# Optimization experiments

Measured on AMD Instinct MI355X. Metric: run time of the kernel, lower is better.

## Reference

```python
import jax, jax.numpy as jnp
import numpy as np

EPS = 1e-6


def setup_inputs() -> dict:
    key = jax.random.key(0)
    kq, kk, kv = jax.random.split(key, 3)
    B, H, S, D = 1, 16, 2048, 64
    q = jax.random.normal(kq, (B, H, S, D), dtype=jnp.float32)
    k = jax.random.normal(kk, (B, H, S, D), dtype=jnp.float32)
    v = jax.random.normal(kv, (B, H, S, D), dtype=jnp.float32)
    return {"q": q, "k": k, "v": v}


def reference(q, k, v):
    # Rebased linear attention: squared scaled QK score, causal mask,
    # normalized by running row-sum (not softmax).
    B, H, S, D = q.shape
    scale = D ** (-0.5)
    # [B,H,S,S] raw scores
    s = jnp.einsum("bhid,bhjd->bhij", q, k) * scale
    s2 = s * s
    causal = jnp.tril(jnp.ones((S, S), dtype=bool))  # k_idx <= q_idx
    s2 = jnp.where(causal, s2, jnp.zeros((), dtype=s2.dtype))
    z = jnp.sum(s2, axis=-1)  # [B,H,S]
    o = jnp.einsum("bhij,bhjd->bhid", s2, v)
    return o / (z[..., None] + EPS)
```

## Files before the change

kernel.cpp:

```cpp
#include <hip/hip_runtime.h>

typedef __attribute__((ext_vector_type(8))) short bf16x8;
typedef __attribute__((ext_vector_type(16))) float f32x16;

#define SLEN 2048
#define DDIM 64
#define NH 16
#define KEPS 1e-6f
#define TILE_B 16384

__device__ __forceinline__ unsigned cvtpk(float lo, float hi) {
    unsigned r;
    asm("v_cvt_pk_bf16_f32 %0, %1, %2" : "=v"(r) : "v"(lo), "v"(hi));
    return r;
}
__device__ __forceinline__ f32x16 mfma32x32(bf16x8 a, bf16x8 b, f32x16 c) {
    return __builtin_amdgcn_mfma_f32_32x32x16_bf16(a, b, c, 0, 0, 0);
}

__global__ void __launch_bounds__(256) prep_kernel(
    const float* __restrict__ K, const float* __restrict__ V, char* __restrict__ WS)
{
    const int b  = blockIdx.x;
    const int h  = b >> 5;
    const int kt = b & 31;
    const int t  = threadIdx.x;
    char* chunk = WS + (size_t)b * TILE_B;

    {
        const int j = t >> 2, ks = t & 3, c16 = ks * 16;
        const float* src = K + ((size_t)h * SLEN + kt * 64 + j) * DDIM + c16;
        float4 a = ((const float4*)src)[0], bb = ((const float4*)src)[1];
        float4 c = ((const float4*)src)[2], d = ((const float4*)src)[3];
        uint4 lo = make_uint4(cvtpk(a.x,a.y), cvtpk(a.z,a.w), cvtpk(bb.x,bb.y), cvtpk(bb.z,bb.w));
        uint4 hi = make_uint4(cvtpk(c.x,c.y), cvtpk(c.z,c.w), cvtpk(d.x,d.y), cvtpk(d.z,d.w));
        *(uint4*)(chunk + ((size_t)((ks*2+0)*64 + j)) * 16) = lo;
        *(uint4*)(chunk + ((size_t)((ks*2+1)*64 + j)) * 16) = hi;
    }
    {
        const int j0 = (t & 15) * 4, d0 = (t >> 4) * 4;
        const float* vs = V + ((size_t)h * SLEN + kt * 64 + j0) * DDIM + d0;
        float4 r0 = *(const float4*)(vs);
        float4 r1 = *(const float4*)(vs + DDIM);
        float4 r2 = *(const float4*)(vs + 2 * DDIM);
        float4 r3 = *(const float4*)(vs + 3 * DDIM);
        char* vbase = chunk + 8192;
        const int cv  = ((j0 >> 4) << 1) | ((j0 >> 3) & 1);
        const int tof = j0 & 7;
#pragma unroll
        for (int c = 0; c < 4; ++c) {
            uint2 pk = make_uint2(
                cvtpk(((const float*)&r0)[c], ((const float*)&r1)[c]),
                cvtpk(((const float*)&r2)[c], ((const float*)&r3)[c]));
            *(uint2*)(vbase + (size_t)(cv * 64 + d0 + c) * 16 + tof * 2) = pk;
        }
    }
}

__global__ void __launch_bounds__(256, 2) attn_main(
    const float* __restrict__ Q, const char* __restrict__ WS, float* __restrict__ O)
{
    __shared__ float red[2][3][64][33];

    const int bid = blockIdx.x;
    const int xcd = bid & 7;
    const int m   = bid >> 3;
    const int h   = ((m & 1) << 3) | xcd;
    const int s   = m >> 1;

    const int tid  = threadIdx.x;
    const int w    = tid >> 6;
    const int lane = tid & 63;
    const int il   = lane & 31;
    const int hi   = lane >> 5;
    const int jb   = w & 1;
    const int e    = w >> 1;

    const float* __restrict__ Qh = Q + (size_t)h * SLEN * DDIM;
    float* __restrict__ Oh = O + (size_t)h * SLEN * DDIM;
    const char* __restrict__ WSh = WS + (size_t)h * 32 * TILE_B;

    const int koff = (hi * 64 + jb * 32 + il) * 16;
    const int voff = 8192 + ((jb * 4 + hi) * 64 + il) * 16;

    auto process = [&](int slice, int phase) {
        const int g    = slice >> 1;
        const int half = slice & 1;
        const int q0   = slice * 32;

        bf16x8 qf[4];
#pragma unroll
        for (int ks = 0; ks < 4; ++ks) {
            const float* src = Qh + (size_t)(q0 + il) * DDIM + ks * 16 + hi * 8;
            float4 a = *reinterpret_cast<const float4*>(src);
            float4 b = *reinterpret_cast<const float4*>(src + 4);
            uint4 uq = make_uint4(cvtpk(a.x, a.y), cvtpk(a.z, a.w),
                                  cvtpk(b.x, b.y), cvtpk(b.z, b.w));
            qf[ks] = *reinterpret_cast<bf16x8*>(&uq);
        }

        f32x16 o0, o1;
#pragma unroll
        for (int rr = 0; rr < 16; ++rr) { o0[rr] = 0.f; o1[rr] = 0.f; }
        float z = 0.f;

        const int ktend = g - ((jb > half) ? 1 : 0);

        if (e <= ktend) {
            const char* kb = WSh + (size_t)e * TILE_B + koff;
            bf16x8 kf0 = *(const bf16x8*)(kb);
            bf16x8 kf1 = *(const bf16x8*)(kb + 2048);
            bf16x8 kf2 = *(const bf16x8*)(kb + 4096);
            bf16x8 kf3 = *(const bf16x8*)(kb + 6144);
            const char* vb = WSh + (size_t)e * TILE_B + voff;
            bf16x8 v00 = *(const bf16x8*)(vb);
            bf16x8 v01 = *(const bf16x8*)(vb + 512);
            bf16x8 v10 = *(const bf16x8*)(vb + 2048);
            bf16x8 v11 = *(const bf16x8*)(vb + 2560);

            for (int kt = e; kt <= ktend; kt += 2) {
                __builtin_amdgcn_s_setprio(1);
                f32x16 sv;
#pragma unroll
                for (int rr = 0; rr < 16; ++rr) sv[rr] = 0.f;
                sv = mfma32x32(kf0, qf[0], sv);
                sv = mfma32x32(kf1, qf[1], sv);
                sv = mfma32x32(kf2, qf[2], sv);
                sv = mfma32x32(kf3, qf[3], sv);
                __builtin_amdgcn_s_setprio(0);

                if (kt + 2 <= ktend) {
                    const char* nb = WSh + (size_t)(kt + 2) * TILE_B + koff;
                    kf0 = *(const bf16x8*)(nb);
                    kf1 = *(const bf16x8*)(nb + 2048);
                    kf2 = *(const bf16x8*)(nb + 4096);
                    kf3 = *(const bf16x8*)(nb + 6144);
                }

                const bool tri = (kt == g) && (jb == half);
#pragma unroll
                for (int rr = 0; rr < 16; ++rr) {
                    float x = sv[rr];
                    x = x * x * 0.015625f;
                    if (tri) {
                        int jl = (rr & 3) + 8 * (rr >> 2) + 4 * hi;
                        if (jl > il) x = 0.f;
                    }
                    sv[rr] = x;
                }
                {
                    float a0 = (sv[0] + sv[1]) + (sv[2] + sv[3]);
                    float a1 = (sv[4] + sv[5]) + (sv[6] + sv[7]);
                    float a2 = (sv[8] + sv[9]) + (sv[10] + sv[11]);
                    float a3 = (sv[12] + sv[13]) + (sv[14] + sv[15]);
                    z += (a0 + a1) + (a2 + a3);
                }

                __builtin_amdgcn_s_setprio(1);
                {
                    unsigned X  = cvtpk(sv[0], sv[1]);
                    unsigned Xp = cvtpk(sv[2], sv[3]);
                    unsigned Y  = cvtpk(sv[4], sv[5]);
                    unsigned Yp = cvtpk(sv[6], sv[7]);
                    asm("v_permlane32_swap_b32 %0, %1" : "+v"(X), "+v"(Y));
                    asm("v_permlane32_swap_b32 %0, %1" : "+v"(Xp), "+v"(Yp));
                    uint4 aw = make_uint4(X, Xp, Y, Yp);
                    bf16x8 pf = *reinterpret_cast<bf16x8*>(&aw);
                    o0 = mfma32x32(pf, v00, o0);
                    o1 = mfma32x32(pf, v01, o1);
                }
                {
                    unsigned X  = cvtpk(sv[8],  sv[9]);
                    unsigned Xp = cvtpk(sv[10], sv[11]);
                    unsigned Y  = cvtpk(sv[12], sv[13]);
                    unsigned Yp = cvtpk(sv[14], sv[15]);
                    asm("v_permlane32_swap_b32 %0, %1" : "+v"(X), "+v"(Y));
                    asm("v_permlane32_swap_b32 %0, %1" : "+v"(Xp), "+v"(Yp));
                    uint4 aw = make_uint4(X, Xp, Y, Yp);
                    bf16x8 pf = *reinterpret_cast<bf16x8*>(&aw);
                    o0 = mfma32x32(pf, v10, o0);
                    o1 = mfma32x32(pf, v11, o1);
                }
                __builtin_amdgcn_s_setprio(0);

                if (kt + 2 <= ktend) {
                    const char* nv = WSh + (size_t)(kt + 2) * TILE_B + voff;
                    v00 = *(const bf16x8*)(nv);
                    v01 = *(const bf16x8*)(nv + 512);
                    v10 = *(const bf16x8*)(nv + 2048);
                    v11 = *(const bf16x8*)(nv + 2560);
                }
            }
        }

        z += __shfl_xor(z, 32);
        if (w != 0) {
            float* r = &red[phase][w - 1][lane][0];
#pragma unroll
            for (int rr = 0; rr < 16; ++rr) { r[rr] = o0[rr]; r[16 + rr] = o1[rr]; }
            r[32] = z;
        }
        __syncthreads();
        if (w == 0) {
#pragma unroll
            for (int pp = 0; pp < 3; ++pp) {
                const float* r = &red[phase][pp][lane][0];
#pragma unroll
                for (int rr = 0; rr < 16; ++rr) { o0[rr] += r[rr]; o1[rr] += r[16 + rr]; }
                z += r[32];
            }
            const float invl = 1.f / (z + KEPS);
#pragma unroll
            for (int rr = 0; rr < 16; ++rr) {
                const int rl = (rr & 3) + 8 * (rr >> 2) + 4 * hi;
                const float inv = __shfl(invl, rl);
                Oh[(size_t)(q0 + rl) * DDIM + il]      = o0[rr] * inv;
                Oh[(size_t)(q0 + rl) * DDIM + 32 + il] = o1[rr] * inv;
            }
        }
    };

    process(s, 0);
    process(63 - s, 1);
}

__global__ void __launch_bounds__(512, 4) attn_fp32(
    const float* __restrict__ Q, const float* __restrict__ K,
    const float* __restrict__ V, float* __restrict__ O)
{
    __shared__ float red[2][3][64][33];
    const int bid = blockIdx.x;
    const int xcd = bid & 7;
    const int m   = bid >> 3;
    const int h   = xcd | ((m & 1) << 3);
    const int c   = m >> 1;
    const int tid  = threadIdx.x;
    const int w    = tid >> 6;
    const int lane = tid & 63;
    const int il   = lane & 31;
    const int hi   = lane >> 5;
    const int msel = w >> 2;
    const int jb   = (w >> 1) & 1;
    const int e    = w & 1;
    const int g    = msel ? (31 - c) : c;
    const int half = msel;
    const int q0   = g * 64 + half * 32;

    const float* Qh = Q + (size_t)h * SLEN * DDIM;
    const float* Kh = K + (size_t)h * SLEN * DDIM;
    const float* Vh = V + (size_t)h * SLEN * DDIM;
    float* Oh = O + (size_t)h * SLEN * DDIM;

    bf16x8 qf[4];
#pragma unroll
    for (int ks = 0; ks < 4; ++ks) {
        const float* src = Qh + (size_t)(q0 + il) * DDIM + ks * 16 + hi * 8;
        float4 a = *reinterpret_cast<const float4*>(src);
        float4 b = *reinterpret_cast<const float4*>(src + 4);
        uint4 uq = make_uint4(cvtpk(a.x, a.y), cvtpk(a.z, a.w),
                              cvtpk(b.x, b.y), cvtpk(b.z, b.w));
        qf[ks] = *reinterpret_cast<bf16x8*>(&uq);
    }
    f32x16 oacc0, oacc1;
#pragma unroll
    for (int rr = 0; rr < 16; ++rr) { oacc0[rr] = 0.f; oacc1[rr] = 0.f; }
    float zacc = 0.f;
    const int ktend = g - ((jb > half) ? 1 : 0);

    for (int kt = e; kt <= ktend; kt += 2) {
        f32x16 sv;
#pragma unroll
        for (int rr = 0; rr < 16; ++rr) sv[rr] = 0.f;
#pragma unroll
        for (int ks = 0; ks < 4; ++ks) {
            const float* src = Kh + (size_t)(kt * 64 + jb * 32 + il) * DDIM + ks * 16 + hi * 8;
            float4 a = *reinterpret_cast<const float4*>(src);
            float4 b = *reinterpret_cast<const float4*>(src + 4);
            uint4 uk = make_uint4(cvtpk(a.x, a.y), cvtpk(a.z, a.w),
                                  cvtpk(b.x, b.y), cvtpk(b.z, b.w));
            sv = mfma32x32(*reinterpret_cast<bf16x8*>(&uk), qf[ks], sv);
        }
        const bool tri = (kt == g) && (jb == half);
#pragma unroll
        for (int rr = 0; rr < 16; ++rr) {
            float x = sv[rr];
            x = x * x * 0.015625f;
            if (tri) {
                int jl = (rr & 3) + 8 * (rr >> 2) + 4 * hi;
                if (jl > il) x = 0.f;
            }
            sv[rr] = x;
            zacc += x;
        }
#pragma unroll
        for (int s16 = 0; s16 < 2; ++s16) {
            unsigned X  = cvtpk(sv[8*s16+0], sv[8*s16+1]);
            unsigned Xp = cvtpk(sv[8*s16+2], sv[8*s16+3]);
            unsigned Y  = cvtpk(sv[8*s16+4], sv[8*s16+5]);
            unsigned Yp = cvtpk(sv[8*s16+6], sv[8*s16+7]);
            asm("v_permlane32_swap_b32 %0, %1" : "+v"(X), "+v"(Y));
            asm("v_permlane32_swap_b32 %0, %1" : "+v"(Xp), "+v"(Yp));
            uint4 aw = make_uint4(X, Xp, Y, Yp);
            bf16x8 pf = *reinterpret_cast<bf16x8*>(&aw);
#pragma unroll
            for (int dt = 0; dt < 2; ++dt) {
                float v8[8];
#pragma unroll
                for (int t = 0; t < 8; ++t)
                    v8[t] = Vh[(size_t)(kt * 64 + (jb * 2 + s16) * 16 + hi * 8 + t) * DDIM + dt * 32 + il];
                uint4 uv = make_uint4(cvtpk(v8[0], v8[1]), cvtpk(v8[2], v8[3]),
                                      cvtpk(v8[4], v8[5]), cvtpk(v8[6], v8[7]));
                bf16x8 vf = *reinterpret_cast<bf16x8*>(&uv);
                if (dt == 0) oacc0 = mfma32x32(pf, vf, oacc0);
                else         oacc1 = mfma32x32(pf, vf, oacc1);
            }
        }
    }

    zacc += __shfl_xor(zacc, 32);
    const int sw = w & 3;
    if (sw != 0) {
        float* r = &red[msel][sw - 1][lane][0];
#pragma unroll
        for (int rr = 0; rr < 16; ++rr) { r[rr] = oacc0[rr]; r[16 + rr] = oacc1[rr]; }
        r[32] = zacc;
    }
    __syncthreads();
    if (sw == 0) {
#pragma unroll
        for (int pp = 0; pp < 3; ++pp) {
            const float* r = &red[msel][pp][lane][0];
#pragma unroll
            for (int rr = 0; rr < 16; ++rr) { oacc0[rr] += r[rr]; oacc1[rr] += r[16 + rr]; }
            zacc += r[32];
        }
        const float invl = 1.f / (zacc + KEPS);
#pragma unroll
        for (int rr = 0; rr < 16; ++rr) {
            const int rl = (rr & 3) + 8 * (rr >> 2) + 4 * hi;
            const float inv = __shfl(invl, rl);
            Oh[(size_t)(q0 + rl) * DDIM + il]      = oacc0[rr] * inv;
            Oh[(size_t)(q0 + rl) * DDIM + 32 + il] = oacc1[rr] * inv;
        }
    }
}

extern "C" void kernel_launch(void* const* d_in, const int* in_sizes, int n_in,
                              void* d_out, int out_size, void* d_ws, size_t ws_size,
                              hipStream_t stream) {
    const float* q = (const float*)d_in[0];
    const float* k = (const float*)d_in[1];
    const float* v = (const float*)d_in[2];
    float* o = (float*)d_out;

    const size_t need = (size_t)NH * 32 * TILE_B;
    if (ws_size >= need) {
        char* ws = (char*)d_ws;
        hipLaunchKernelGGL(prep_kernel, dim3(NH * 32), dim3(256), 0, stream, k, v, ws);
        hipLaunchKernelGGL(attn_main, dim3(512), dim3(256), 0, stream, q, ws, o);
    } else {
        hipLaunchKernelGGL(attn_fp32, dim3(512), dim3(512), 0, stream, q, k, v, o);
    }
}
```

Baseline: 30.99 us.

## Fuse paired query slices into one KV loop sharing K/V fragment loads

Each block now processes two 32-row query slices (one near the start and a mirrored one near the end) in a single pass over KV tiles instead of two sequential passes. Each K/V fragment load serves both slices, and the A slice's MFMAs are gated by a predicate, which cuts redundant global loads and lets more independent MFMAs overlap. The block-to-head/slice mapping also changes from the XCD-interleaved scheme to a plain h = bid & 15 layout. The cost is roughly double the accumulator and Q register state, which may pressure occupancy under launch_bounds(256,2), plus an extra barrier in the reduction.

```diff
diff --git a/kernel.cpp b/kernel.cpp
--- a/kernel.cpp
+++ b/kernel.cpp
@@ -60,13 +60,13 @@
 __global__ void __launch_bounds__(256, 2) attn_main(
     const float* __restrict__ Q, const char* __restrict__ WS, float* __restrict__ O)
 {
-    __shared__ float red[2][3][64][33];
+    __shared__ float red[3][64][33];
 
     const int bid = blockIdx.x;
-    const int xcd = bid & 7;
-    const int m   = bid >> 3;
-    const int h   = ((m & 1) << 3) | xcd;
-    const int s   = m >> 1;
+    const int h   = bid & 15;
+    const int u   = bid >> 4;
+    const int pr    = (u < 16) ? u : (15 - (u - 16));
+    const int halfb = u >> 4;
 
     const int tid  = threadIdx.x;
     const int w    = tid >> 6;
@@ -76,6 +76,11 @@
     const int jb   = w & 1;
     const int e    = w >> 1;
 
+    const int gA = pr;
+    const int gB = 31 - pr;
+    const int qA0 = gA * 64 + halfb * 32;
+    const int qB0 = gB * 64 + halfb * 32;
+
     const float* __restrict__ Qh = Q + (size_t)h * SLEN * DDIM;
     float* __restrict__ Oh = O + (size_t)h * SLEN * DDIM;
     const char* __restrict__ WSh = WS + (size_t)h * 32 * TILE_B;
@@ -83,145 +88,186 @@
     const int koff = (hi * 64 + jb * 32 + il) * 16;
     const int voff = 8192 + ((jb * 4 + hi) * 64 + il) * 16;
 
-    auto process = [&](int slice, int phase) {
-        const int g    = slice >> 1;
-        const int half = slice & 1;
-        const int q0   = slice * 32;
-
-        bf16x8 qf[4];
-#pragma unroll
-        for (int ks = 0; ks < 4; ++ks) {
-            const float* src = Qh + (size_t)(q0 + il) * DDIM + ks * 16 + hi * 8;
+    bf16x8 qA[4], qB[4];
+#pragma unroll
+    for (int ks = 0; ks < 4; ++ks) {
+        {
+            const float* src = Qh + (size_t)(qA0 + il) * DDIM + ks * 16 + hi * 8;
             float4 a = *reinterpret_cast<const float4*>(src);
             float4 b = *reinterpret_cast<const float4*>(src + 4);
             uint4 uq = make_uint4(cvtpk(a.x, a.y), cvtpk(a.z, a.w),
                                   cvtpk(b.x, b.y), cvtpk(b.z, b.w));
-            qf[ks] = *reinterpret_cast<bf16x8*>(&uq);
-        }
-
-        f32x16 o0, o1;
-#pragma unroll
-        for (int rr = 0; rr < 16; ++rr) { o0[rr] = 0.f; o1[rr] = 0.f; }
-        float z = 0.f;
-
-        const int ktend = g - ((jb > half) ? 1 : 0);
-
-        if (e <= ktend) {
-            const char* kb = WSh + (size_t)e * TILE_B + koff;
-            bf16x8 kf0 = *(const bf16x8*)(kb);
-            bf16x8 kf1 = *(const bf16x8*)(kb + 2048);
-            bf16x8 kf2 = *(const bf16x8*)(kb + 4096);
-            bf16x8 kf3 = *(const bf16x8*)(kb + 6144);
-            const char* vb = WSh + (size_t)e * TILE_B + voff;
-            bf16x8 v00 = *(const bf16x8*)(vb);
-            bf16x8 v01 = *(const bf16x8*)(vb + 512);
-            bf16x8 v10 = *(const bf16x8*)(vb + 2048);
-            bf16x8 v11 = *(const bf16x8*)(vb + 2560);
-
-            for (int kt = e; kt <= ktend; kt += 2) {
-                __builtin_amdgcn_s_setprio(1);
-                f32x16 sv;
-#pragma unroll
-                for (int rr = 0; rr < 16; ++rr) sv[rr] = 0.f;
-                sv = mfma32x32(kf0, qf[0], sv);
-                sv = mfma32x32(kf1, qf[1], sv);
-                sv = mfma32x32(kf2, qf[2], sv);
-                sv = mfma32x32(kf3, qf[3], sv);
-                __builtin_amdgcn_s_setprio(0);
-
-                if (kt + 2 <= ktend) {
-                    const char* nb = WSh + (size_t)(kt + 2) * TILE_B + koff;
-                    kf0 = *(const bf16x8*)(nb);
-                    kf1 = *(const bf16x8*)(nb + 2048);
-                    kf2 = *(const bf16x8*)(nb + 4096);
-                    kf3 = *(const bf16x8*)(nb + 6144);
-                }
-
-                const bool tri = (kt == g) && (jb == half);
-#pragma unroll
-                for (int rr = 0; rr < 16; ++rr) {
-                    float x = sv[rr];
-                    x = x * x * 0.015625f;
-                    if (tri) {
-                        int jl = (rr & 3) + 8 * (rr >> 2) + 4 * hi;
-                        if (jl > il) x = 0.f;
-                    }
-                    sv[rr] = x;
-                }
-                {
-                    float a0 = (sv[0] + sv[1]) + (sv[2] + sv[3]);
-                    float a1 = (sv[4] + sv[5]) + (sv[6] + sv[7]);
-                    float a2 = (sv[8] + sv[9]) + (sv[10] + sv[11]);
-                    float a3 = (sv[12] + sv[13]) + (sv[14] + sv[15]);
-                    z += (a0 + a1) + (a2 + a3);
-                }
-
-                __builtin_amdgcn_s_setprio(1);
-                {
-                    unsigned X  = cvtpk(sv[0], sv[1]);
-                    unsigned Xp = cvtpk(sv[2], sv[3]);
-                    unsigned Y  = cvtpk(sv[4], sv[5]);
-                    unsigned Yp = cvtpk(sv[6], sv[7]);
-                    asm("v_permlane32_swap_b32 %0, %1" : "+v"(X), "+v"(Y));
-                    asm("v_permlane32_swap_b32 %0, %1" : "+v"(Xp), "+v"(Yp));
-                    uint4 aw = make_uint4(X, Xp, Y, Yp);
-                    bf16x8 pf = *reinterpret_cast<bf16x8*>(&aw);
-                    o0 = mfma32x32(pf, v00, o0);
-                    o1 = mfma32x32(pf, v01, o1);
-                }
-                {
-                    unsigned X  = cvtpk(sv[8],  sv[9]);
-                    unsigned Xp = cvtpk(sv[10], sv[11]);
-                    unsigned Y  = cvtpk(sv[12], sv[13]);
-                    unsigned Yp = cvtpk(sv[14], sv[15]);
-                    asm("v_permlane32_swap_b32 %0, %1" : "+v"(X), "+v"(Y));
-                    asm("v_permlane32_swap_b32 %0, %1" : "+v"(Xp), "+v"(Yp));
-                    uint4 aw = make_uint4(X, Xp, Y, Yp);
-                    bf16x8 pf = *reinterpret_cast<bf16x8*>(&aw);
-                    o0 = mfma32x32(pf, v10, o0);
-                    o1 = mfma32x32(pf, v11, o1);
-                }
-                __builtin_amdgcn_s_setprio(0);
-
-                if (kt + 2 <= ktend) {
-                    const char* nv = WSh + (size_t)(kt + 2) * TILE_B + voff;
-                    v00 = *(const bf16x8*)(nv);
-                    v01 = *(const bf16x8*)(nv + 512);
-                    v10 = *(const bf16x8*)(nv + 2048);
-                    v11 = *(const bf16x8*)(nv + 2560);
-                }
+            qA[ks] = *reinterpret_cast<bf16x8*>(&uq);
+        }
+        {
+            const float* src = Qh + (size_t)(qB0 + il) * DDIM + ks * 16 + hi * 8;
+            float4 a = *reinterpret_cast<const float4*>(src);
+            float4 b = *reinterpret_cast<const float4*>(src + 4);
+            uint4 uq = make_uint4(cvtpk(a.x, a.y), cvtpk(a.z, a.w),
+                                  cvtpk(b.x, b.y), cvtpk(b.z, b.w));
+            qB[ks] = *reinterpret_cast<bf16x8*>(&uq);
+        }
+    }
+
+    f32x16 oa0, oa1, ob0, ob1;
+#pragma unroll
+    for (int rr = 0; rr < 16; ++rr) { oa0[rr] = 0.f; oa1[rr] = 0.f; ob0[rr] = 0.f; ob1[rr] = 0.f; }
+    float za = 0.f, zb = 0.f;
+
+    const int ktendA = gA - ((jb > halfb) ? 1 : 0);
+    const int ktendB = gB - ((jb > halfb) ? 1 : 0);
+
+    auto finish = [&](f32x16& sv, bool tri, f32x16& o0, f32x16& o1, float& z,
+                      bf16x8 v00, bf16x8 v01, bf16x8 v10, bf16x8 v11) {
+#pragma unroll
+        for (int rr = 0; rr < 16; ++rr) {
+            float x = sv[rr];
+            x = x * x * 0.015625f;
+            if (tri) {
+                int jl = (rr & 3) + 8 * (rr >> 2) + 4 * hi;
+                if (jl > il) x = 0.f;
             }
-        }
-
-        z += __shfl_xor(z, 32);
-        if (w != 0) {
-            float* r = &red[phase][w - 1][lane][0];
-#pragma unroll
-            for (int rr = 0; rr < 16; ++rr) { r[rr] = o0[rr]; r[16 + rr] = o1[rr]; }
-            r[32] = z;
-        }
-        __syncthreads();
-        if (w == 0) {
-#pragma unroll
-            for (int pp = 0; pp < 3; ++pp) {
-                const float* r = &red[phase][pp][lane][0];
-#pragma unroll
-                for (int rr = 0; rr < 16; ++rr) { o0[rr] += r[rr]; o1[rr] += r[16 + rr]; }
-                z += r[32];
+            sv[rr] = x;
+        }
+        {
+            float a0 = (sv[0] + sv[1]) + (sv[2] + sv[3]);
+            float a1 = (sv[4] + sv[5]) + (sv[6] + sv[7]);
+            float a2 = (sv[8] + sv[9]) + (sv[10] + sv[11]);
+            float a3 = (sv[12] + sv[13]) + (sv[14] + sv[15]);
+            z += (a0 + a1) + (a2 + a3);
+        }
+        {
+            unsigned X  = cvtpk(sv[0], sv[1]);
+            unsigned Xp = cvtpk(sv[2], sv[3]);
+            unsigned Y  = cvtpk(sv[4], sv[5]);
+            unsigned Yp = cvtpk(sv[6], sv[7]);
+            asm("v_permlane32_swap_b32 %0, %1" : "+v"(X), "+v"(Y));
+            asm("v_permlane32_swap_b32 %0, %1" : "+v"(Xp), "+v"(Yp));
+            uint4 aw = make_uint4(X, Xp, Y, Yp);
+            bf16x8 pf = *reinterpret_cast<bf16x8*>(&aw);
+            o0 = mfma32x32(pf, v00, o0);
+            o1 = mfma32x32(pf, v01, o1);
+        }
+        {
+            unsigned X  = cvtpk(sv[8],  sv[9]);
+            unsigned Xp = cvtpk(sv[10], sv[11]);
+            unsigned Y  = cvtpk(sv[12], sv[13]);
+            unsigned Yp = cvtpk(sv[14], sv[15]);
+            asm("v_permlane32_swap_b32 %0, %1" : "+v"(X), "+v"(Y));
+            asm("v_permlane32_swap_b32 %0, %1" : "+v"(Xp), "+v"(Yp));
+            uint4 aw = make_uint4(X, Xp, Y, Yp);
+            bf16x8 pf = *reinterpret_cast<bf16x8*>(&aw);
+            o0 = mfma32x32(pf, v10, o0);
+            o1 = mfma32x32(pf, v11, o1);
+        }
+    };
+
+    {
+        const char* kb = WSh + (size_t)e * TILE_B + koff;
+        bf16x8 kf0 = *(const bf16x8*)(kb);
+        bf16x8 kf1 = *(const bf16x8*)(kb + 2048);
+        bf16x8 kf2 = *(const bf16x8*)(kb + 4096);
+        bf16x8 kf3 = *(const bf16x8*)(kb + 6144);
+        const char* vb = WSh + (size_t)e * TILE_B + voff;
+        bf16x8 v00 = *(const bf16x8*)(vb);
+        bf16x8 v01 = *(const bf16x8*)(vb + 512);
+        bf16x8 v10 = *(const bf16x8*)(vb + 2048);
+        bf16x8 v11 = *(const bf16x8*)(vb + 2560);
+
+        for (int kt = e; kt <= ktendB; kt += 2) {
+            const bool actA = (kt <= ktendA);
+            __builtin_amdgcn_s_setprio(1);
+            f32x16 sB;
+#pragma unroll
+            for (int rr = 0; rr < 16; ++rr) sB[rr] = 0.f;
+            sB = mfma32x32(kf0, qB[0], sB);
+            sB = mfma32x32(kf1, qB[1], sB);
+            sB = mfma32x32(kf2, qB[2], sB);
+            sB = mfma32x32(kf3, qB[3], sB);
+            f32x16 sA;
+            if (actA) {
+#pragma unroll
+                for (int rr = 0; rr < 16; ++rr) sA[rr] = 0.f;
+                sA = mfma32x32(kf0, qA[0], sA);
+                sA = mfma32x32(kf1, qA[1], sA);
+                sA = mfma32x32(kf2, qA[2], sA);
+                sA = mfma32x32(kf3, qA[3], sA);
             }
-            const float invl = 1.f / (z + KEPS);
-#pragma unroll
-            for (int rr = 0; rr < 16; ++rr) {
-                const int rl = (rr & 3) + 8 * (rr >> 2) + 4 * hi;
-                const float inv = __shfl(invl, rl);
-                Oh[(size_t)(q0 + rl) * DDIM + il]      = o0[rr] * inv;
-                Oh[(size_t)(q0 + rl) * DDIM + 32 + il] = o1[rr] * inv;
-            }
-        }
-    };
-
-    process(s, 0);
-    process(63 - s, 1);
+            __builtin_amdgcn_s_setprio(0);
+
+            const int ktn = (kt + 2 <= ktendB) ? kt + 2 : kt;
+            const char* nb = WSh + (size_t)ktn * TILE_B + koff;
+            kf0 = *(const bf16x8*)(nb);
+            kf1 = *(const bf16x8*)(nb + 2048);
+            kf2 = *(const bf16x8*)(nb + 4096);
+            kf3 = *(const bf16x8*)(nb + 6144);
+
+            __builtin_amdgcn_s_setprio(1);
+            finish(sB, (kt == gB) && (jb == halfb), ob0, ob1, zb, v00, v01, v10, v11);
+            if (actA)
+                finish(sA, (kt == gA) && (jb == halfb), oa0, oa1, za, v00, v01, v10, v11);
+            __builtin_amdgcn_s_setprio(0);
+
+            const char* nv = WSh + (size_t)ktn * TILE_B + voff;
+            v00 = *(const bf16x8*)(nv);
+            v01 = *(const bf16x8*)(nv + 512);
+            v10 = *(const bf16x8*)(nv + 2048);
+            v11 = *(const bf16x8*)(nv + 2560);
+        }
+    }
+
+    za += __shfl_xor(za, 32);
+    zb += __shfl_xor(zb, 32);
+
+    if (w != 0) {
+        float* r = &red[w - 1][lane][0];
+#pragma unroll
+        for (int rr = 0; rr < 16; ++rr) { r[rr] = oa0[rr]; r[16 + rr] = oa1[rr]; }
+        r[32] = za;
+    }
+    __syncthreads();
+    if (w == 0) {
+#pragma unroll
+        for (int pp = 0; pp < 3; ++pp) {
+            const float* r = &red[pp][lane][0];
+#pragma unroll
+            for (int rr = 0; rr < 16; ++rr) { oa0[rr] += r[rr]; oa1[rr] += r[16 + rr]; }
+            za += r[32];
+        }
+        const float invl = 1.f / (za + KEPS);
+#pragma unroll
+        for (int rr = 0; rr < 16; ++rr) {
+            const int rl = (rr & 3) + 8 * (rr >> 2) + 4 * hi;
+            const float inv = __shfl(invl, rl);
+            Oh[(size_t)(qA0 + rl) * DDIM + il]      = oa0[rr] * inv;
+            Oh[(size_t)(qA0 + rl) * DDIM + 32 + il] = oa1[rr] * inv;
+        }
+    }
+    __syncthreads();
+    if (w != 0) {
+        float* r = &red[w - 1][lane][0];
+#pragma unroll
+        for (int rr = 0; rr < 16; ++rr) { r[rr] = ob0[rr]; r[16 + rr] = ob1[rr]; }
+        r[32] = zb;
+    }
+    __syncthreads();
+    if (w == 0) {
+#pragma unroll
+        for (int pp = 0; pp < 3; ++pp) {
+            const float* r = &red[pp][lane][0];
+#pragma unroll
+            for (int rr = 0; rr < 16; ++rr) { ob0[rr] += r[rr]; ob1[rr] += r[16 + rr]; }
+            zb += r[32];
+        }
+        const float invl = 1.f / (zb + KEPS);
+#pragma unroll
+        for (int rr = 0; rr < 16; ++rr) {
+            const int rl = (rr & 3) + 8 * (rr >> 2) + 4 * hi;
+            const float inv = __shfl(invl, rl);
+            Oh[(size_t)(qB0 + rl) * DDIM + il]      = ob0[rr] * inv;
+            Oh[(size_t)(qB0 + rl) * DDIM + 32 + il] = ob1[rr] * inv;
+        }
+    }
 }
 
 __global__ void __launch_bounds__(512, 4) attn_fp32(
```

Result: slower. 32.87 us (+6.1%).

## Stage K/V tiles through double-buffered LDS with async global-to-LDS loads

Applied to the files above, without the earlier changes.

Rewrites the main attention kernel so each block handles one 64-row query group per head and shares K/V tiles across all four waves. Tiles are streamed into a double-buffered shared-memory area with global_load_lds, replacing per-wave direct global loads. Work is split across two query halves times two key halves instead of strided key tiles. Block-to-work mapping changes from a slice pairing within one block to 512 blocks with mirrored causal lengths, and the V packing layout in the prep kernel changes to match. This trades register prefetch for LDS reuse and adds a barrier per key tile. It also drops the occupancy hint of two blocks per CU.

```diff
diff --git a/kernel.cpp b/kernel.cpp
--- a/kernel.cpp
+++ b/kernel.cpp
@@ -16,6 +16,11 @@
 }
 __device__ __forceinline__ f32x16 mfma32x32(bf16x8 a, bf16x8 b, f32x16 c) {
     return __builtin_amdgcn_mfma_f32_32x32x16_bf16(a, b, c, 0, 0, 0);
+}
+__device__ __forceinline__ void gload16(const void* g, void* l) {
+    __builtin_amdgcn_global_load_lds(
+        (const __attribute__((address_space(1))) unsigned*)g,
+        (__attribute__((address_space(3))) unsigned*)l, 16, 0, 0);
 }
 
 __global__ void __launch_bounds__(256) prep_kernel(
@@ -45,7 +50,7 @@
         float4 r2 = *(const float4*)(vs + 2 * DDIM);
         float4 r3 = *(const float4*)(vs + 3 * DDIM);
         char* vbase = chunk + 8192;
-        const int cv  = ((j0 >> 4) << 1) | ((j0 >> 3) & 1);
+        const int cv  = j0 >> 3;
         const int tof = j0 & 7;
 #pragma unroll
         for (int c = 0; c < 4; ++c) {
@@ -57,199 +62,29 @@
     }
 }
 
-__global__ void __launch_bounds__(256, 2) attn_main(
+__global__ void __launch_bounds__(256) attn_main(
     const float* __restrict__ Q, const char* __restrict__ WS, float* __restrict__ O)
 {
-    __shared__ float red[2][3][64][33];
+    __shared__ __align__(16) char smem[2][TILE_B];
 
     const int bid = blockIdx.x;
-    const int xcd = bid & 7;
-    const int m   = bid >> 3;
-    const int h   = ((m & 1) << 3) | xcd;
-    const int s   = m >> 1;
+    const int h   = bid & 15;
+    const int u   = bid >> 4;
+    const int g   = (u < 16) ? u : (47 - u);
 
     const int tid  = threadIdx.x;
     const int w    = tid >> 6;
     const int lane = tid & 63;
     const int il   = lane & 31;
     const int hi   = lane >> 5;
-    const int jb   = w & 1;
-    const int e    = w >> 1;
+    const int qhalf = w >> 1;
+    const int jb    = w & 1;
+
+    const int q0 = g * 64 + qhalf * 32;
 
     const float* __restrict__ Qh = Q + (size_t)h * SLEN * DDIM;
     float* __restrict__ Oh = O + (size_t)h * SLEN * DDIM;
     const char* __restrict__ WSh = WS + (size_t)h * 32 * TILE_B;
-
-    const int koff = (hi * 64 + jb * 32 + il) * 16;
-    const int voff = 8192 + ((jb * 4 + hi) * 64 + il) * 16;
-
-    auto process = [&](int slice, int phase) {
-        const int g    = slice >> 1;
-        const int half = slice & 1;
-        const int q0   = slice * 32;
-
-        bf16x8 qf[4];
-#pragma unroll
-        for (int ks = 0; ks < 4; ++ks) {
-            const float* src = Qh + (size_t)(q0 + il) * DDIM + ks * 16 + hi * 8;
-            float4 a = *reinterpret_cast<const float4*>(src);
-            float4 b = *reinterpret_cast<const float4*>(src + 4);
-            uint4 uq = make_uint4(cvtpk(a.x, a.y), cvtpk(a.z, a.w),
-                                  cvtpk(b.x, b.y), cvtpk(b.z, b.w));
-            qf[ks] = *reinterpret_cast<bf16x8*>(&uq);
-        }
-
-        f32x16 o0, o1;
-#pragma unroll
-        for (int rr = 0; rr < 16; ++rr) { o0[rr] = 0.f; o1[rr] = 0.f; }
-        float z = 0.f;
-
-        const int ktend = g - ((jb > half) ? 1 : 0);
-
-        if (e <= ktend) {
-            const char* kb = WSh + (size_t)e * TILE_B + koff;
-            bf16x8 kf0 = *(const bf16x8*)(kb);
-            bf16x8 kf1 = *(const bf16x8*)(kb + 2048);
-            bf16x8 kf2 = *(const bf16x8*)(kb + 4096);
-            bf16x8 kf3 = *(const bf16x8*)(kb + 6144);
-            const char* vb = WSh + (size_t)e * TILE_B + voff;
-            bf16x8 v00 = *(const bf16x8*)(vb);
-            bf16x8 v01 = *(const bf16x8*)(vb + 512);
-            bf16x8 v10 = *(const bf16x8*)(vb + 2048);
-            bf16x8 v11 = *(const bf16x8*)(vb + 2560);
-
-            for (int kt = e; kt <= ktend; kt += 2) {
-                __builtin_amdgcn_s_setprio(1);
-                f32x16 sv;
-#pragma unroll
-                for (int rr = 0; rr < 16; ++rr) sv[rr] = 0.f;
-                sv = mfma32x32(kf0, qf[0], sv);
-                sv = mfma32x32(kf1, qf[1], sv);
-                sv = mfma32x32(kf2, qf[2], sv);
-                sv = mfma32x32(kf3, qf[3], sv);
-                __builtin_amdgcn_s_setprio(0);
-
-                if (kt + 2 <= ktend) {
-                    const char* nb = WSh + (size_t)(kt + 2) * TILE_B + koff;
-                    kf0 = *(const bf16x8*)(nb);
-                    kf1 = *(const bf16x8*)(nb + 2048);
-                    kf2 = *(const bf16x8*)(nb + 4096);
-                    kf3 = *(const bf16x8*)(nb + 6144);
-                }
-
-                const bool tri = (kt == g) && (jb == half);
-#pragma unroll
-                for (int rr = 0; rr < 16; ++rr) {
-                    float x = sv[rr];
-                    x = x * x * 0.015625f;
-                    if (tri) {
-                        int jl = (rr & 3) + 8 * (rr >> 2) + 4 * hi;
-                        if (jl > il) x = 0.f;
-                    }
-                    sv[rr] = x;
-                }
-                {
-                    float a0 = (sv[0] + sv[1]) + (sv[2] + sv[3]);
-                    float a1 = (sv[4] + sv[5]) + (sv[6] + sv[7]);
-                    float a2 = (sv[8] + sv[9]) + (sv[10] + sv[11]);
-                    float a3 = (sv[12] + sv[13]) + (sv[14] + sv[15]);
-                    z += (a0 + a1) + (a2 + a3);
-                }
-
-                __builtin_amdgcn_s_setprio(1);
-                {
-                    unsigned X  = cvtpk(sv[0], sv[1]);
-                    unsigned Xp = cvtpk(sv[2], sv[3]);
-                    unsigned Y  = cvtpk(sv[4], sv[5]);
-                    unsigned Yp = cvtpk(sv[6], sv[7]);
-                    asm("v_permlane32_swap_b32 %0, %1" : "+v"(X), "+v"(Y));
-                    asm("v_permlane32_swap_b32 %0, %1" : "+v"(Xp), "+v"(Yp));
-                    uint4 aw = make_uint4(X, Xp, Y, Yp);
-                    bf16x8 pf = *reinterpret_cast<bf16x8*>(&aw);
-                    o0 = mfma32x32(pf, v00, o0);
-                    o1 = mfma32x32(pf, v01, o1);
-                }
-                {
-                    unsigned X  = cvtpk(sv[8],  sv[9]);
-                    unsigned Xp = cvtpk(sv[10], sv[11]);
-                    unsigned Y  = cvtpk(sv[12], sv[13]);
-                    unsigned Yp = cvtpk(sv[14], sv[15]);
-                    asm("v_permlane32_swap_b32 %0, %1" : "+v"(X), "+v"(Y));
-                    asm("v_permlane32_swap_b32 %0, %1" : "+v"(Xp), "+v"(Yp));
-                    uint4 aw = make_uint4(X, Xp, Y, Yp);
-                    bf16x8 pf = *reinterpret_cast<bf16x8*>(&aw);
-                    o0 = mfma32x32(pf, v10, o0);
-                    o1 = mfma32x32(pf, v11, o1);
-                }
-                __builtin_amdgcn_s_setprio(0);
-
-                if (kt + 2 <= ktend) {
-                    const char* nv = WSh + (size_t)(kt + 2) * TILE_B + voff;
-                    v00 = *(const bf16x8*)(nv);
-                    v01 = *(const bf16x8*)(nv + 512);
-                    v10 = *(const bf16x8*)(nv + 2048);
-                    v11 = *(const bf16x8*)(nv + 2560);
-                }
-            }
-        }
-
-        z += __shfl_xor(z, 32);
-        if (w != 0) {
-            float* r = &red[phase][w - 1][lane][0];
-#pragma unroll
-            for (int rr = 0; rr < 16; ++rr) { r[rr] = o0[rr]; r[16 + rr] = o1[rr]; }
-            r[32] = z;
-        }
-        __syncthreads();
-        if (w == 0) {
-#pragma unroll
-            for (int pp = 0; pp < 3; ++pp) {
-                const float* r = &red[phase][pp][lane][0];
-#pragma unroll
-                for (int rr = 0; rr < 16; ++rr) { o0[rr] += r[rr]; o1[rr] += r[16 + rr]; }
-                z += r[32];
-            }
-            const float invl = 1.f / (z + KEPS);
-#pragma unroll
-            for (int rr = 0; rr < 16; ++rr) {
-                const int rl = (rr & 3) + 8 * (rr >> 2) + 4 * hi;
-                const float inv = __shfl(invl, rl);
-                Oh[(size_t)(q0 + rl) * DDIM + il]      = o0[rr] * inv;
-                Oh[(size_t)(q0 + rl) * DDIM + 32 + il] = o1[rr] * inv;
-            }
-        }
-    };
-
-    process(s, 0);
-    process(63 - s, 1);
-}
-
-__global__ void __launch_bounds__(512, 4) attn_fp32(
-    const float* __restrict__ Q, const float* __restrict__ K,
-    const float* __restrict__ V, float* __restrict__ O)
-{
-    __shared__ float red[2][3][64][33];
-    const int bid = blockIdx.x;
-    const int xcd = bid & 7;
-    const int m   = bid >> 3;
-    const int h   = xcd | ((m & 1) << 3);
-    const int c   = m >> 1;
-    const int tid  = threadIdx.x;
-    const int w    = tid >> 6;
-    const int lane = tid & 63;
-    const int il   = lane & 31;
-    const int hi   = lane >> 5;
-    const int msel = w >> 2;
-    const int jb   = (w >> 1) & 1;
-    const int e    = w & 1;
-    const int g    = msel ? (31 - c) : c;
-    const int half = msel;
-    const int q0   = g * 64 + half * 32;
-
-    const float* Qh = Q + (size_t)h * SLEN * DDIM;
-    const float* Kh = K + (size_t)h * SLEN * DDIM;
-    const float* Vh = V + (size_t)h * SLEN * DDIM;
-    float* Oh = O + (size_t)h * SLEN * DDIM;
 
     bf16x8 qf[4];
 #pragma unroll
@@ -261,13 +96,169 @@
                               cvtpk(b.x, b.y), cvtpk(b.z, b.w));
         qf[ks] = *reinterpret_cast<bf16x8*>(&uq);
     }
-    f32x16 oacc0, oacc1;
-#pragma unroll
-    for (int rr = 0; rr < 16; ++rr) { oacc0[rr] = 0.f; oacc1[rr] = 0.f; }
-    float zacc = 0.f;
-    const int ktend = g - ((jb > half) ? 1 : 0);
-
-    for (int kt = e; kt <= ktend; kt += 2) {
+
+    f32x16 o0, o1;
+#pragma unroll
+    for (int rr = 0; rr < 16; ++rr) { o0[rr] = 0.f; o1[rr] = 0.f; }
+    float z = 0.f;
+
+    auto stage = [&](int buf, int kt) {
+        const char* gs = WSh + (size_t)kt * TILE_B + w * 4096 + lane * 16;
+        char* ls = &smem[buf][w * 4096];
+#pragma unroll
+        for (int i = 0; i < 4; ++i)
+            gload16(gs + i * 1024, ls + i * 1024);
+    };
+
+    const int kbase = (jb * 32 + il) * 16;
+    const int vbase = 8192 + (jb * 4 + hi) * 1024 + il * 16;
+
+    const int ktend = g - ((jb > qhalf) ? 1 : 0);
+
+    stage(0, 0);
+    __syncthreads();
+
+    for (int kt = 0; kt <= g; ++kt) {
+        const int cur = kt & 1;
+        if (kt < g) stage(cur ^ 1, kt + 1);
+
+        if (kt <= ktend) {
+            const char* base = smem[cur];
+            bf16x8 kf0 = *(const bf16x8*)(base + 0 * 1024 + hi * 1024 + kbase);
+            bf16x8 kf1 = *(const bf16x8*)(base + 2 * 1024 + hi * 1024 + kbase);
+            bf16x8 kf2 = *(const bf16x8*)(base + 4 * 1024 + hi * 1024 + kbase);
+            bf16x8 kf3 = *(const bf16x8*)(base + 6 * 1024 + hi * 1024 + kbase);
+
+            __builtin_amdgcn_s_setprio(1);
+            f32x16 sv;
+#pragma unroll
+            for (int rr = 0; rr < 16; ++rr) sv[rr] = 0.f;
+            sv = mfma32x32(kf0, qf[0], sv);
+            sv = mfma32x32(kf1, qf[1], sv);
+            sv = mfma32x32(kf2, qf[2], sv);
+            sv = mfma32x32(kf3, qf[3], sv);
+            __builtin_amdgcn_s_setprio(0);
+
+            const bool tri = (kt == g) && (jb == qhalf);
+#pragma unroll
+            for (int rr = 0; rr < 16; ++rr) {
+                float x = sv[rr];
+                x = x * x * 0.015625f;
+                if (tri) {
+                    int jl = (rr & 3) + 8 * (rr >> 2) + 4 * hi;
+                    if (jl > il) x = 0.f;
+                }
+                sv[rr] = x;
+            }
+            {
+                float a0 = (sv[0] + sv[1]) + (sv[2] + sv[3]);
+                float a1 = (sv[4] + sv[5]) + (sv[6] + sv[7]);
+                float a2 = (sv[8] + sv[9]) + (sv[10] + sv[11]);
+                float a3 = (sv[12] + sv[13]) + (sv[14] + sv[15]);
+                z += (a0 + a1) + (a2 + a3);
+            }
+
+            __builtin_amdgcn_s_setprio(1);
+            {
+                unsigned X  = cvtpk(sv[0], sv[1]);
+                unsigned Xp = cvtpk(sv[2], sv[3]);
+                unsigned Y  = cvtpk(sv[4], sv[5]);
+                unsigned Yp = cvtpk(sv[6], sv[7]);
+                asm("v_permlane32_swap_b32 %0, %1" : "+v"(X), "+v"(Y));
+                asm("v_permlane32_swap_b32 %0, %1" : "+v"(Xp), "+v"(Yp));
+                uint4 aw = make_uint4(X, Xp, Y, Yp);
+                bf16x8 pf = *reinterpret_cast<bf16x8*>(&aw);
+                bf16x8 va = *(const bf16x8*)(base + vbase + 0 * 2048 + 0 * 512);
+                bf16x8 vb = *(const bf16x8*)(base + vbase + 0 * 2048 + 1 * 512);
+                o0 = mfma32x32(pf, va, o0);
+                o1 = mfma32x32(pf, vb, o1);
+            }
+            {
+                unsigned X  = cvtpk(sv[8],  sv[9]);
+                unsigned Xp = cvtpk(sv[10], sv[11]);
+                unsigned Y  = cvtpk(sv[12], sv[13]);
+                unsigned Yp = cvtpk(sv[14], sv[15]);
+                asm("v_permlane32_swap_b32 %0, %1" : "+v"(X), "+v"(Y));
+                asm("v_permlane32_swap_b32 %0, %1" : "+v"(Xp), "+v"(Yp));
+                uint4 aw = make_uint4(X, Xp, Y, Yp);
+                bf16x8 pf = *reinterpret_cast<bf16x8*>(&aw);
+                bf16x8 va = *(const bf16x8*)(base + vbase + 1 * 2048 + 0 * 512);
+                bf16x8 vb = *(const bf16x8*)(base + vbase + 1 * 2048 + 1 * 512);
+                o0 = mfma32x32(pf, va, o0);
+                o1 = mfma32x32(pf, vb, o1);
+            }
+            __builtin_amdgcn_s_setprio(0);
+        }
+
+        __syncthreads();
+    }
+
+    z += __shfl_xor(z, 32);
+    float* red = (float*)smem;
+    if (jb == 1) {
+        float* r = red + (size_t)((qhalf * 64 + lane) * 33);
+#pragma unroll
+        for (int rr = 0; rr < 16; ++rr) { r[rr] = o0[rr]; r[16 + rr] = o1[rr]; }
+        r[32] = z;
+    }
+    __syncthreads();
+    if (jb == 0) {
+        const float* r = red + (size_t)((qhalf * 64 + lane) * 33);
+#pragma unroll
+        for (int rr = 0; rr < 16; ++rr) { o0[rr] += r[rr]; o1[rr] += r[16 + rr]; }
+        z += r[32];
+
+        const float invl = 1.f / (z + KEPS);
+#pragma unroll
+        for (int rr = 0; rr < 16; ++rr) {
+            const int rl = (rr & 3) + 8 * (rr >> 2) + 4 * hi;
+            const float inv = __shfl(invl, rl);
+            Oh[(size_t)(q0 + rl) * DDIM + il]      = o0[rr] * inv;
+            Oh[(size_t)(q0 + rl) * DDIM + 32 + il] = o1[rr] * inv;
+        }
+    }
+}
+
+__global__ void __launch_bounds__(256) attn_fp32(
+    const float* __restrict__ Q, const float* __restrict__ K,
+    const float* __restrict__ V, float* __restrict__ O)
+{
+    __shared__ float red[2][64][33];
+    const int bid = blockIdx.x;
+    const int h   = bid & 15;
+    const int u   = bid >> 4;
+    const int g   = (u < 16) ? u : (47 - u);
+    const int tid  = threadIdx.x;
+    const int w    = tid >> 6;
+    const int lane = tid & 63;
+    const int il   = lane & 31;
+    const int hi   = lane >> 5;
+    const int qhalf = w >> 1;
+    const int jb    = w & 1;
+    const int q0 = g * 64 + qhalf * 32;
+
+    const float* Qh = Q + (size_t)h * SLEN * DDIM;
+    const float* Kh = K + (size_t)h * SLEN * DDIM;
+    const float* Vh = V + (size_t)h * SLEN * DDIM;
+    float* Oh = O + (size_t)h * SLEN * DDIM;
+
+    bf16x8 qf[4];
+#pragma unroll
+    for (int ks = 0; ks < 4; ++ks) {
+        const float* src = Qh + (size_t)(q0 + il) * DDIM + ks * 16 + hi * 8;
+        float4 a = *reinterpret_cast<const float4*>(src);
+        float4 b = *reinterpret_cast<const float4*>(src + 4);
+        uint4 uq = make_uint4(cvtpk(a.x, a.y), cvtpk(a.z, a.w),
+                              cvtpk(b.x, b.y), cvtpk(b.z, b.w));
+        qf[ks] = *reinterpret_cast<bf16x8*>(&uq);
+    }
+    f32x16 o0, o1;
+#pragma unroll
+    for (int rr = 0; rr < 16; ++rr) { o0[rr] = 0.f; o1[rr] = 0.f; }
+    float z = 0.f;
+    const int ktend = g - ((jb > qhalf) ? 1 : 0);
+
+    for (int kt = 0; kt <= ktend; ++kt) {
         f32x16 sv;
 #pragma unroll
         for (int rr = 0; rr < 16; ++rr) sv[rr] = 0.f;
@@ -280,7 +271,7 @@
                                   cvtpk(b.x, b.y), cvtpk(b.z, b.w));
             sv = mfma32x32(*reinterpret_cast<bf16x8*>(&uk), qf[ks], sv);
         }
-        const bool tri = (kt == g) && (jb == half);
+        const bool tri = (kt == g) && (jb == qhalf);
 #pragma unroll
         for (int rr = 0; rr < 16; ++rr) {
             float x = sv[rr];
@@ -290,7 +281,7 @@
                 if (jl > il) x = 0.f;
             }
             sv[rr] = x;
-            zacc += x;
+            z += x;
         }
 #pragma unroll
         for (int s16 = 0; s16 < 2; ++s16) {
@@ -307,40 +298,36 @@
                 float v8[8];
 #pragma unroll
                 for (int t = 0; t < 8; ++t)
-                    v8[t] = Vh[(size_t)(kt * 64 + (jb * 2 + s16) * 16 + hi * 8 + t) * DDIM + dt * 32 + il];
+                    v8[t] = Vh[(size_t)(kt * 64 + jb * 32 + s16 * 16 + hi * 8 + t) * DDIM + dt * 32 + il];
                 uint4 uv = make_uint4(cvtpk(v8[0], v8[1]), cvtpk(v8[2], v8[3]),
                                       cvtpk(v8[4], v8[5]), cvtpk(v8[6], v8[7]));
                 bf16x8 vf = *reinterpret_cast<bf16x8*>(&uv);
-                if (dt == 0) oacc0 = mfma32x32(pf, vf, oacc0);
-                else         oacc1 = mfma32x32(pf, vf, oacc1);
-            }
-        }
-    }
-
-    zacc += __shfl_xor(zacc, 32);
-    const int sw = w & 3;
-    if (sw != 0) {
-        float* r = &red[msel][sw - 1][lane][0];
-#pragma unroll
-        for (int rr = 0; rr < 16; ++rr) { r[rr] = oacc0[rr]; r[16 + rr] = oacc1[rr]; }
-        r[32] = zacc;
+                if (dt == 0) o0 = mfma32x32(pf, vf, o0);
+                else         o1 = mfma32x32(pf, vf, o1);
+            }
+        }
+    }
+
+    z += __shfl_xor(z, 32);
+    if (jb == 1) {
+        float* r = &red[qhalf][lane][0];
+#pragma unroll
+        for (int rr = 0; rr < 16; ++rr) { r[rr] = o0[rr]; r[16 + rr] = o1[rr]; }
+        r[32] = z;
     }
     __syncthreads();
-    if (sw == 0) {
-#pragma unroll
-        for (int pp = 0; pp < 3; ++pp) {
-            const float* r = &red[msel][pp][lane][0];
-#pragma unroll
-            for (int rr = 0; rr < 16; ++rr) { oacc0[rr] += r[rr]; oacc1[rr] += r[16 + rr]; }
-            zacc += r[32];
-        }
-        const float invl = 1.f / (zacc + KEPS);
+    if (jb == 0) {
+        const float* r = &red[qhalf][lane][0];
+#pragma unroll
+        for (int rr = 0; rr < 16; ++rr) { o0[rr] += r[rr]; o1[rr] += r[16 + rr]; }
+        z += r[32];
+        const float invl = 1.f / (z + KEPS);
 #pragma unroll
         for (int rr = 0; rr < 16; ++rr) {
             const int rl = (rr & 3) + 8 * (rr >> 2) + 4 * hi;
             const float inv = __shfl(invl, rl);
-            Oh[(size_t)(q0 + rl) * DDIM + il]      = oacc0[rr] * inv;
-            Oh[(size_t)(q0 + rl) * DDIM + 32 + il] = oacc1[rr] * inv;
+            Oh[(size_t)(q0 + rl) * DDIM + il]      = o0[rr] * inv;
+            Oh[(size_t)(q0 + rl) * DDIM + 32 + il] = o1[rr] * inv;
         }
     }
 }
@@ -359,6 +346,6 @@
         hipLaunchKernelGGL(prep_kernel, dim3(NH * 32), dim3(256), 0, stream, k, v, ws);
         hipLaunchKernelGGL(attn_main, dim3(512), dim3(256), 0, stream, q, ws, o);
     } else {
-        hipLaunchKernelGGL(attn_fp32, dim3(512), dim3(512), 0, stream, q, k, v, o);
-    }
-}
+        hipLaunchKernelGGL(attn_fp32, dim3(512), dim3(256), 0, stream, q, k, v, o);
+    }
+}
```

After: 33.04 us. 1.07x slower.
